# Optimization experiments

Hardware: AMD Instinct MI355X
Metric: run time of the kernel (lower is better)

The kernel has to match this reference:

```python
import jax, jax.numpy as jnp
import numpy as np

B, L, T = 8, 4096, 128
D_H, D_G, D_PROJ = 1024, 256, 256


def setup_inputs() -> dict:
    key = jax.random.key(0)
    k1, k2, k3, k4, k5 = jax.random.split(key, 5)
    H = jax.random.normal(k1, (B, L, D_H), dtype=jnp.float32)
    G = jax.random.normal(k2, (B, T, D_G), dtype=jnp.float32)
    mask = jax.random.randint(k3, (B, L), 0, 2) == 1  # True = masked out
    Wk = jax.random.normal(k4, (D_H, D_PROJ), dtype=jnp.float32) * 0.02
    Wq = jax.random.normal(k5, (D_G, D_PROJ), dtype=jnp.float32) * 0.02
    return {"H": H, "G": G, "mask": mask, "Wk": Wk, "Wq": Wq}


def reference(H, G, mask, Wk, Wq):
    scale = D_PROJ ** (-0.5)
    K = jnp.einsum('bld,dp->blp', H, Wk)          # [B, L, d_proj]
    Q = jnp.einsum('btd,dp->btp', G, Wq)          # [B, T, d_proj]
    logits = jnp.einsum('btp,blp->btl', Q, K) * scale  # [B, T, L]
    logits = jnp.where(mask[:, None, :], -jnp.inf, logits)
    alpha = jax.nn.softmax(logits, axis=-1)       # [B, T, L]
    Z = jnp.einsum('btl,bld->btd', alpha, H)      # [B, T, d_h]
    return Z
```

## Files before the change

kernel.cpp:

```cpp
#include <hip/hip_runtime.h>
#include <hip/hip_bf16.h>
#include <math.h>

#define B_  8
#define L_  4096
#define T_  128
#define DH  1024
#define DG  256
#define DP  256
#define BK  64
#define ZCH 8

typedef short bf16x8 __attribute__((ext_vector_type(8)));
typedef float f32x4  __attribute__((ext_vector_type(4)));

#define AS1(p) ((const __attribute__((address_space(1))) void*)(p))
#define AS3(p) ((__attribute__((address_space(3))) void*)(p))

__device__ __forceinline__ unsigned short f2bf(float f) {
    unsigned u = __float_as_uint(f);
    unsigned r = (u + 0x7FFFu + ((u >> 16) & 1u)) >> 16;
    return (unsigned short)r;
}

__global__ __launch_bounds__(256) void wct_kernel(const float* __restrict__ Wk,
                                                  const float* __restrict__ Wq,
                                                  unsigned short* __restrict__ Wct) {
    __shared__ __attribute__((aligned(16))) unsigned short As[128 * BK];
    __shared__ __attribute__((aligned(16))) unsigned short Bs[64 * BK];
    const int n0 = blockIdx.x * 64, m0 = blockIdx.y * 128;
    const int tid = threadIdx.x, wave = tid >> 6, lane = tid & 63;
    const int lm = lane & 15, quad = lane >> 4;
    const int wm = wave >> 1, wn = wave & 1;
    const int bc = (tid & 15) * 4, br = tid >> 4;
    f32x4 acc[4][2] = {};

    for (int k0 = 0; k0 < DP; k0 += BK) {
        #pragma unroll
        for (int s = 0; s < 8; ++s) {
            const int row = br + s * 16;
            const float4 v = *(const float4*)(Wk + (size_t)(m0 + row) * DP + k0 + bc);
            ushort4 p; p.x = f2bf(v.x); p.y = f2bf(v.y); p.z = f2bf(v.z); p.w = f2bf(v.w);
            *(ushort4*)(&As[row * BK + bc]) = p;
        }
        #pragma unroll
        for (int s = 0; s < 4; ++s) {
            const int row = br + s * 16;
            const float4 v = *(const float4*)(Wq + (size_t)(n0 + row) * DP + k0 + bc);
            ushort4 p; p.x = f2bf(v.x); p.y = f2bf(v.y); p.z = f2bf(v.z); p.w = f2bf(v.w);
            *(ushort4*)(&Bs[row * BK + bc]) = p;
        }
        __syncthreads();
        #pragma unroll
        for (int ks = 0; ks < 2; ++ks) {
            bf16x8 a[4], bf[2];
            #pragma unroll
            for (int i = 0; i < 4; ++i)
                a[i] = *(const bf16x8*)(&As[(wm * 64 + i * 16 + lm) * BK + ks * 32 + quad * 8]);
            #pragma unroll
            for (int j = 0; j < 2; ++j)
                bf[j] = *(const bf16x8*)(&Bs[(wn * 32 + j * 16 + lm) * BK + ks * 32 + quad * 8]);
            #pragma unroll
            for (int i = 0; i < 4; ++i)
                #pragma unroll
                for (int j = 0; j < 2; ++j)
                    acc[i][j] = __builtin_amdgcn_mfma_f32_16x16x32_bf16(a[i], bf[j], acc[i][j], 0, 0, 0);
        }
        __syncthreads();
    }
    unsigned short* Cb = Wct + (size_t)m0 * DG + n0;
    #pragma unroll
    for (int i = 0; i < 4; ++i)
        #pragma unroll
        for (int j = 0; j < 2; ++j)
            #pragma unroll
            for (int r = 0; r < 4; ++r)
                Cb[(size_t)(wm * 64 + i * 16 + quad * 4 + r) * DG + wn * 32 + j * 16 + lm] =
                    f2bf(acc[i][j][r] * 0.0625f);
}

__global__ __launch_bounds__(256) void qproj_kernel(const float* __restrict__ G,
                                                    const unsigned short* __restrict__ Wct,
                                                    unsigned short* __restrict__ Qk) {
    __shared__ __attribute__((aligned(16))) unsigned short As[128 * BK];
    __shared__ __attribute__((aligned(16))) unsigned short Bs[64 * BK];
    const int n0 = blockIdx.x * 64, m0 = blockIdx.y * 128;
    const int tid = threadIdx.x, wave = tid >> 6, lane = tid & 63;
    const int lm = lane & 15, quad = lane >> 4;
    const int wm = wave >> 1, wn = wave & 1;
    const int bc = (tid & 15) * 4, br = tid >> 4;
    const int ar = lane >> 3, akb = (lane & 7) * 8;
    f32x4 acc[4][2] = {};

    for (int k0 = 0; k0 < DG; k0 += BK) {
        #pragma unroll
        for (int s = 0; s < 8; ++s) {
            const int row = br + s * 16;
            const float4 v = *(const float4*)(G + (size_t)(m0 + row) * DG + k0 + bc);
            ushort4 p; p.x = f2bf(v.x); p.y = f2bf(v.y); p.z = f2bf(v.z); p.w = f2bf(v.w);
            *(ushort4*)(&As[row * BK + bc]) = p;
        }
        #pragma unroll
        for (int s = 0; s < 2; ++s) {
            const int rowb = s * 32 + wave * 8;
            const unsigned short* gp = Wct + (size_t)(n0 + rowb + ar) * DG + k0 + akb;
            __builtin_amdgcn_global_load_lds(AS1(gp), AS3(&Bs[rowb * BK]), 16, 0, 0);
        }
        __syncthreads();
        #pragma unroll
        for (int ks = 0; ks < 2; ++ks) {
            bf16x8 a[4], bf[2];
            #pragma unroll
            for (int i = 0; i < 4; ++i)
                a[i] = *(const bf16x8*)(&As[(wm * 64 + i * 16 + lm) * BK + ks * 32 + quad * 8]);
            #pragma unroll
            for (int j = 0; j < 2; ++j)
                bf[j] = *(const bf16x8*)(&Bs[(wn * 32 + j * 16 + lm) * BK + ks * 32 + quad * 8]);
            #pragma unroll
            for (int i = 0; i < 4; ++i)
                #pragma unroll
                for (int j = 0; j < 2; ++j)
                    acc[i][j] = __builtin_amdgcn_mfma_f32_16x16x32_bf16(a[i], bf[j], acc[i][j], 0, 0, 0);
        }
        __syncthreads();
    }
    unsigned short* Cb = Qk + (size_t)m0 * DH + n0;
    #pragma unroll
    for (int i = 0; i < 4; ++i)
        #pragma unroll
        for (int j = 0; j < 2; ++j)
            #pragma unroll
            for (int r = 0; r < 4; ++r)
                Cb[(size_t)(wm * 64 + i * 16 + quad * 4 + r) * DH + wn * 32 + j * 16 + lm] =
                    f2bf(acc[i][j][r]);
}

__global__ __launch_bounds__(256, 2) void fusedsm_kernel(const unsigned short* __restrict__ Qk,
                                                         const float* __restrict__ H,
                                                         const int* __restrict__ mask,
                                                         unsigned short* __restrict__ alpha,
                                                         float* __restrict__ rowsum) {
    __shared__ __attribute__((aligned(16))) unsigned short As[T_ * BK];
    __shared__ __attribute__((aligned(16))) unsigned short Bs[64 * BK];
    __shared__ float rs[T_];
    const int l0 = blockIdx.x * 64, b = blockIdx.y;
    const int tid = threadIdx.x, wave = tid >> 6, lane = tid & 63;
    const unsigned short* Ab = Qk + (size_t)b * T_ * DH;
    const float*          Hb = H + ((size_t)b * L_ + l0) * DH;

    const int lm = lane & 15, quad = lane >> 4;
    const int wm = wave >> 1, wn = wave & 1;
    f32x4 acc[4][2] = {};
    const int ar = lane >> 3, akb = (lane & 7) * 8;
    const int bc = (tid & 15) * 4, br = tid >> 4;

    if (tid < T_) rs[tid] = 0.f;

    for (int k0 = 0; k0 < DH; k0 += BK) {
        #pragma unroll
        for (int s = 0; s < 4; ++s) {
            const int rowb = s * 32 + wave * 8;
            const unsigned short* gp = Ab + (size_t)(rowb + ar) * DH + k0 + akb;
            __builtin_amdgcn_global_load_lds(AS1(gp), AS3(&As[rowb * BK]), 16, 0, 0);
        }
        #pragma unroll
        for (int s = 0; s < 4; ++s) {
            const int row = br + s * 16;
            const float4 v = *(const float4*)(Hb + (size_t)row * DH + k0 + bc);
            ushort4 p; p.x = f2bf(v.x); p.y = f2bf(v.y); p.z = f2bf(v.z); p.w = f2bf(v.w);
            *(ushort4*)(&Bs[row * BK + bc]) = p;
        }
        __syncthreads();
        #pragma unroll
        for (int ks = 0; ks < 2; ++ks) {
            bf16x8 a[4], bf[2];
            #pragma unroll
            for (int i = 0; i < 4; ++i)
                a[i] = *(const bf16x8*)(&As[(wm * 64 + i * 16 + lm) * BK + ks * 32 + quad * 8]);
            #pragma unroll
            for (int j = 0; j < 2; ++j)
                bf[j] = *(const bf16x8*)(&Bs[(wn * 32 + j * 16 + lm) * BK + ks * 32 + quad * 8]);
            #pragma unroll
            for (int i = 0; i < 4; ++i)
                #pragma unroll
                for (int j = 0; j < 2; ++j)
                    acc[i][j] = __builtin_amdgcn_mfma_f32_16x16x32_bf16(a[i], bf[j], acc[i][j], 0, 0, 0);
        }
        __syncthreads();
    }

    const int c0 = l0 + wn * 32 + lm;
    const int mk0 = mask[(size_t)b * L_ + c0];
    const int mk1 = mask[(size_t)b * L_ + c0 + 16];
    unsigned short* Arow = alpha + (size_t)b * T_ * L_ + l0 + wn * 32 + lm;
    #pragma unroll
    for (int i = 0; i < 4; ++i) {
        #pragma unroll
        for (int r = 0; r < 4; ++r) {
            const int row = wm * 64 + i * 16 + quad * 4 + r;
            float e0 = mk0 ? 0.f : __expf(acc[i][0][r]);
            float e1 = mk1 ? 0.f : __expf(acc[i][1][r]);
            Arow[(size_t)row * L_]      = f2bf(e0);
            Arow[(size_t)row * L_ + 16] = f2bf(e1);
            float part = e0 + e1;
            part += __shfl_xor(part, 1, 64);
            part += __shfl_xor(part, 2, 64);
            part += __shfl_xor(part, 4, 64);
            part += __shfl_xor(part, 8, 64);
            if (lm == 0) atomicAdd(&rs[row], part);
        }
    }
    __syncthreads();
    if (tid < T_) atomicAdd(&rowsum[(size_t)b * T_ + tid], rs[tid]);
}

__global__ __launch_bounds__(256, 2) void z_kernel(const unsigned short* __restrict__ alpha,
                                                   const float* __restrict__ H,
                                                   float* __restrict__ part) {
    __shared__ __attribute__((aligned(16))) unsigned short As[T_ * BK];
    __shared__ __attribute__((aligned(16))) unsigned B32[128 * 32];
    const int d0 = blockIdx.x * 128, b = blockIdx.y, ch = blockIdx.z;
    const int tid = threadIdx.x, wave = tid >> 6, lane = tid & 63;
    const int Lc = L_ / ZCH;
    const unsigned short* Ab = alpha + (size_t)b * T_ * L_ + ch * Lc;
    const float*          Hb = H + ((size_t)b * L_ + ch * Lc) * DH + d0;

    const int lm = lane & 15, quad = lane >> 4;
    const int wm = wave >> 1, wn = wave & 1;
    f32x4 acc[4][4] = {};
    const int ar = lane >> 3, akb = (lane & 7) * 8;
    const int dg = tid & 15, lph = tid >> 4;

    for (int k0 = 0; k0 < Lc; k0 += BK) {
        #pragma unroll
        for (int s = 0; s < 4; ++s) {
            const int rowb = s * 32 + wave * 8;
            const unsigned short* gp = Ab + (size_t)(rowb + ar) * L_ + k0 + akb;
            __builtin_amdgcn_global_load_lds(AS1(gp), AS3(&As[rowb * BK]), 16, 0, 0);
        }
        {
            const float* r = Hb + (size_t)(k0 + 4 * lph) * DH + dg * 8;
            float v[4][8];
            #pragma unroll
            for (int rr = 0; rr < 4; ++rr) {
                const float4 a = *(const float4*)(r + (size_t)rr * DH);
                const float4 c = *(const float4*)(r + (size_t)rr * DH + 4);
                v[rr][0] = a.x; v[rr][1] = a.y; v[rr][2] = a.z; v[rr][3] = a.w;
                v[rr][4] = c.x; v[rr][5] = c.y; v[rr][6] = c.z; v[rr][7] = c.w;
            }
            const int lp0 = 2 * lph;
            #pragma unroll
            for (int i = 0; i < 8; ++i) {
                const int d   = dg * 8 + i;
                const int rot = ((i + (dg & 7)) << 2) & 31;
                B32[d * 32 + ((lp0 + rot) & 31)] =
                    (unsigned)f2bf(v[0][i]) | ((unsigned)f2bf(v[1][i]) << 16);
                B32[d * 32 + ((lp0 + 1 + rot) & 31)] =
                    (unsigned)f2bf(v[2][i]) | ((unsigned)f2bf(v[3][i]) << 16);
            }
        }
        __syncthreads();
        #pragma unroll
        for (int ks = 0; ks < 2; ++ks) {
            bf16x8 a[4], bf[4];
            #pragma unroll
            for (int i = 0; i < 4; ++i)
                a[i] = *(const bf16x8*)(&As[(wm * 64 + i * 16 + lm) * BK + ks * 32 + quad * 8]);
            #pragma unroll
            for (int j = 0; j < 4; ++j) {
                const int d   = wn * 64 + j * 16 + lm;
                const int rot = (((d & 7) + ((d >> 3) & 7)) << 2) & 31;
                bf[j] = *(const bf16x8*)(&B32[d * 32 + ((ks * 16 + quad * 4 + rot) & 31)]);
            }
            #pragma unroll
            for (int i = 0; i < 4; ++i)
                #pragma unroll
                for (int j = 0; j < 4; ++j)
                    acc[i][j] = __builtin_amdgcn_mfma_f32_16x16x32_bf16(a[i], bf[j], acc[i][j], 0, 0, 0);
        }
        __syncthreads();
    }
    float* Cb = part + (((size_t)ch * B_ + b) * T_) * DH + d0;
    #pragma unroll
    for (int i = 0; i < 4; ++i)
        #pragma unroll
        for (int j = 0; j < 4; ++j)
            #pragma unroll
            for (int r = 0; r < 4; ++r)
                Cb[(size_t)(wm * 64 + i * 16 + quad * 4 + r) * DH + wn * 64 + j * 16 + lm] = acc[i][j][r];
}

__global__ __launch_bounds__(256) void zreduce_kernel(const float* __restrict__ p,
                                                      const float* __restrict__ rowsum,
                                                      float* __restrict__ Z) {
    const size_t n = (size_t)B_ * T_ * DH;
    const size_t i = ((size_t)blockIdx.x * 256 + threadIdx.x) * 4;
    const int row = (int)(i >> 10);
    const float inv = 1.0f / rowsum[row];
    float4 o = {0.f, 0.f, 0.f, 0.f};
    #pragma unroll
    for (int c = 0; c < ZCH; ++c) {
        const float4 a = *(const float4*)(p + (size_t)c * n + i);
        o.x += a.x; o.y += a.y; o.z += a.z; o.w += a.w;
    }
    o.x *= inv; o.y *= inv; o.z *= inv; o.w *= inv;
    *(float4*)(Z + i) = o;
}

extern "C" void kernel_launch(void* const* d_in, const int* in_sizes, int n_in,
                              void* d_out, int out_size, void* d_ws, size_t ws_size,
                              hipStream_t stream) {
    const float* H    = (const float*)d_in[0];
    const float* G    = (const float*)d_in[1];
    const int*   mask = (const int*)d_in[2];
    const float* Wk   = (const float*)d_in[3];
    const float* Wq   = (const float*)d_in[4];
    float* Z = (float*)d_out;

    char* ws = (char*)d_ws;
    unsigned short* Wct    = (unsigned short*)ws;
    unsigned short* Qk     = (unsigned short*)(ws + ((size_t)1 << 20));
    unsigned short* alpha  = (unsigned short*)(ws + ((size_t)4 << 20));
    float*          rowsum = (float*)(ws + ((size_t)13 << 20));
    float*          zpart  = (float*)(ws + ((size_t)14 << 20));

    hipMemsetAsync(rowsum, 0, (size_t)B_ * T_ * sizeof(float), stream);
    wct_kernel<<<dim3(DG / 64, DH / 128), 256, 0, stream>>>(Wk, Wq, Wct);
    qproj_kernel<<<dim3(DH / 64, (B_ * T_) / 128), 256, 0, stream>>>(G, Wct, Qk);
    fusedsm_kernel<<<dim3(L_ / 64, B_), 256, 0, stream>>>(Qk, H, mask, alpha, rowsum);
    z_kernel<<<dim3(DH / 128, B_, ZCH), 256, 0, stream>>>(alpha, H, zpart);
    zreduce_kernel<<<(B_ * T_ * DH / 4) / 256, 256, 0, stream>>>(zpart, rowsum, Z);
}
```

Before: 280.4 us.

## Cache bf16 copy of H in softmax kernel, fuse split-L reduction via atomics

The softmax/logit kernel now writes the bf16-converted H tile to a workspace buffer as it stages it. The Z GEMM then reads this half-size copy instead of re-reading fp32 H and converting it again. The separate partial-sum reduction kernel is removed: each split-L chunk scales its partial by the inverse row sum and atomically adds into a zeroed Z. Block indices are also remapped so neighbouring blocks share batch and chunk data. The cost is an extra 64 MB of writes in the softmax kernel, an added memset of Z, float atomics contending on 8 chunks per element, and a summation order that is no longer deterministic.

```diff
diff --git a/kernel.cpp b/kernel.cpp
--- a/kernel.cpp
+++ b/kernel.cpp
@@ -13,6 +13,7 @@
 
 typedef short bf16x8 __attribute__((ext_vector_type(8)));
 typedef float f32x4  __attribute__((ext_vector_type(4)));
+typedef unsigned short u16x8 __attribute__((ext_vector_type(8)));
 
 #define AS1(p) ((const __attribute__((address_space(1))) void*)(p))
 #define AS3(p) ((__attribute__((address_space(3))) void*)(p))
@@ -139,14 +140,17 @@
                                                          const float* __restrict__ H,
                                                          const int* __restrict__ mask,
                                                          unsigned short* __restrict__ alpha,
-                                                         float* __restrict__ rowsum) {
+                                                         float* __restrict__ rowsum,
+                                                         unsigned short* __restrict__ H16) {
     __shared__ __attribute__((aligned(16))) unsigned short As[T_ * BK];
     __shared__ __attribute__((aligned(16))) unsigned short Bs[64 * BK];
     __shared__ float rs[T_];
-    const int l0 = blockIdx.x * 64, b = blockIdx.y;
+    const int blin = blockIdx.x + (L_ / 64) * blockIdx.y;
+    const int b = blin & 7, l0 = (blin >> 3) * 64;
     const int tid = threadIdx.x, wave = tid >> 6, lane = tid & 63;
     const unsigned short* Ab = Qk + (size_t)b * T_ * DH;
     const float*          Hb = H + ((size_t)b * L_ + l0) * DH;
+    unsigned short*     H16b = H16 + ((size_t)b * L_ + l0) * DH;
 
     const int lm = lane & 15, quad = lane >> 4;
     const int wm = wave >> 1, wn = wave & 1;
@@ -167,8 +171,9 @@
         for (int s = 0; s < 4; ++s) {
             const int row = br + s * 16;
             const float4 v = *(const float4*)(Hb + (size_t)row * DH + k0 + bc);
-            ushort4 p; p.x = f2bf(v.x); p.y = f2bf(v.y); p.z = f2bf(v.z); p.w = f2bf(v.w);
-            *(ushort4*)(&Bs[row * BK + bc]) = p;
+            ushort4 pk; pk.x = f2bf(v.x); pk.y = f2bf(v.y); pk.z = f2bf(v.z); pk.w = f2bf(v.w);
+            *(ushort4*)(&Bs[row * BK + bc]) = pk;
+            *(ushort4*)(H16b + (size_t)row * DH + k0 + bc) = pk;
         }
         __syncthreads();
         #pragma unroll
@@ -215,15 +220,18 @@
 }
 
 __global__ __launch_bounds__(256, 2) void z_kernel(const unsigned short* __restrict__ alpha,
-                                                   const float* __restrict__ H,
-                                                   float* __restrict__ part) {
+                                                   const unsigned short* __restrict__ H16,
+                                                   const float* __restrict__ rowsum,
+                                                   float* __restrict__ Z) {
     __shared__ __attribute__((aligned(16))) unsigned short As[T_ * BK];
     __shared__ __attribute__((aligned(16))) unsigned B32[128 * 32];
-    const int d0 = blockIdx.x * 128, b = blockIdx.y, ch = blockIdx.z;
+    const int blin = blockIdx.x + 8 * (blockIdx.y + 8 * blockIdx.z);
+    const int ch = blin & 7, rest = blin >> 3;
+    const int b = rest & 7, d0 = (rest >> 3) * 128;
     const int tid = threadIdx.x, wave = tid >> 6, lane = tid & 63;
     const int Lc = L_ / ZCH;
     const unsigned short* Ab = alpha + (size_t)b * T_ * L_ + ch * Lc;
-    const float*          Hb = H + ((size_t)b * L_ + ch * Lc) * DH + d0;
+    const unsigned short* Hb = H16 + ((size_t)b * L_ + ch * Lc) * DH + d0;
 
     const int lm = lane & 15, quad = lane >> 4;
     const int wm = wave >> 1, wn = wave & 1;
@@ -239,24 +247,20 @@
             __builtin_amdgcn_global_load_lds(AS1(gp), AS3(&As[rowb * BK]), 16, 0, 0);
         }
         {
-            const float* r = Hb + (size_t)(k0 + 4 * lph) * DH + dg * 8;
-            float v[4][8];
-            #pragma unroll
-            for (int rr = 0; rr < 4; ++rr) {
-                const float4 a = *(const float4*)(r + (size_t)rr * DH);
-                const float4 c = *(const float4*)(r + (size_t)rr * DH + 4);
-                v[rr][0] = a.x; v[rr][1] = a.y; v[rr][2] = a.z; v[rr][3] = a.w;
-                v[rr][4] = c.x; v[rr][5] = c.y; v[rr][6] = c.z; v[rr][7] = c.w;
-            }
+            const unsigned short* r = Hb + (size_t)(k0 + 4 * lph) * DH + dg * 8;
+            u16x8 u[4];
+            #pragma unroll
+            for (int rr = 0; rr < 4; ++rr)
+                u[rr] = *(const u16x8*)(r + (size_t)rr * DH);
             const int lp0 = 2 * lph;
             #pragma unroll
             for (int i = 0; i < 8; ++i) {
                 const int d   = dg * 8 + i;
                 const int rot = ((i + (dg & 7)) << 2) & 31;
                 B32[d * 32 + ((lp0 + rot) & 31)] =
-                    (unsigned)f2bf(v[0][i]) | ((unsigned)f2bf(v[1][i]) << 16);
+                    (unsigned)u[0][i] | ((unsigned)u[1][i] << 16);
                 B32[d * 32 + ((lp0 + 1 + rot) & 31)] =
-                    (unsigned)f2bf(v[2][i]) | ((unsigned)f2bf(v[3][i]) << 16);
+                    (unsigned)u[2][i] | ((unsigned)u[3][i] << 16);
             }
         }
         __syncthreads();
@@ -280,31 +284,19 @@
         }
         __syncthreads();
     }
-    float* Cb = part + (((size_t)ch * B_ + b) * T_) * DH + d0;
+    float* Zb = Z + ((size_t)b * T_) * DH + d0;
+    const float* rsb = rowsum + (size_t)b * T_;
     #pragma unroll
-    for (int i = 0; i < 4; ++i)
-        #pragma unroll
-        for (int j = 0; j < 4; ++j)
-            #pragma unroll
-            for (int r = 0; r < 4; ++r)
-                Cb[(size_t)(wm * 64 + i * 16 + quad * 4 + r) * DH + wn * 64 + j * 16 + lm] = acc[i][j][r];
-}
-
-__global__ __launch_bounds__(256) void zreduce_kernel(const float* __restrict__ p,
-                                                      const float* __restrict__ rowsum,
-                                                      float* __restrict__ Z) {
-    const size_t n = (size_t)B_ * T_ * DH;
-    const size_t i = ((size_t)blockIdx.x * 256 + threadIdx.x) * 4;
-    const int row = (int)(i >> 10);
-    const float inv = 1.0f / rowsum[row];
-    float4 o = {0.f, 0.f, 0.f, 0.f};
-    #pragma unroll
-    for (int c = 0; c < ZCH; ++c) {
-        const float4 a = *(const float4*)(p + (size_t)c * n + i);
-        o.x += a.x; o.y += a.y; o.z += a.z; o.w += a.w;
-    }
-    o.x *= inv; o.y *= inv; o.z *= inv; o.w *= inv;
-    *(float4*)(Z + i) = o;
+    for (int i = 0; i < 4; ++i) {
+        #pragma unroll
+        for (int r = 0; r < 4; ++r) {
+            const int row = wm * 64 + i * 16 + quad * 4 + r;
+            const float inv = 1.0f / rsb[row];
+            #pragma unroll
+            for (int j = 0; j < 4; ++j)
+                atomicAdd(&Zb[(size_t)row * DH + wn * 64 + j * 16 + lm], acc[i][j][r] * inv);
+        }
+    }
 }
 
 extern "C" void kernel_launch(void* const* d_in, const int* in_sizes, int n_in,
@@ -322,12 +314,12 @@
     unsigned short* Qk     = (unsigned short*)(ws + ((size_t)1 << 20));
     unsigned short* alpha  = (unsigned short*)(ws + ((size_t)4 << 20));
     float*          rowsum = (float*)(ws + ((size_t)13 << 20));
-    float*          zpart  = (float*)(ws + ((size_t)14 << 20));
+    unsigned short* H16    = (unsigned short*)(ws + ((size_t)14 << 20));
 
     hipMemsetAsync(rowsum, 0, (size_t)B_ * T_ * sizeof(float), stream);
+    hipMemsetAsync(Z, 0, (size_t)B_ * T_ * DH * sizeof(float), stream);
     wct_kernel<<<dim3(DG / 64, DH / 128), 256, 0, stream>>>(Wk, Wq, Wct);
     qproj_kernel<<<dim3(DH / 64, (B_ * T_) / 128), 256, 0, stream>>>(G, Wct, Qk);
-    fusedsm_kernel<<<dim3(L_ / 64, B_), 256, 0, stream>>>(Qk, H, mask, alpha, rowsum);
-    z_kernel<<<dim3(DH / 128, B_, ZCH), 256, 0, stream>>>(alpha, H, zpart);
-    zreduce_kernel<<<(B_ * T_ * DH / 4) / 256, 256, 0, stream>>>(zpart, rowsum, Z);
-}
+    fusedsm_kernel<<<dim3(L_ / 64, B_), 256, 0, stream>>>(Qk, H, mask, alpha, rowsum, H16);
+    z_kernel<<<dim3(DH / 128, B_, ZCH), 256, 0, stream>>>(alpha, H16, rowsum, Z);
+}
```

Result: slower. 306.5 us (+9.3%).
